# Performance work log

Hardware: AMD Instinct MI355X
Metric: run time of the kernel (lower is better)

Reference implementation:

```python
import jax, jax.numpy as jnp
import numpy as np

N = 100000      # nodes
E = 1600000     # edges (before self-loops)
IN = 256        # input features
HID = 128       # hidden channels
HEADS = 8
C = HID // HEADS  # per-head channels = 16
L = 3           # num GAT layers
EPS = 1e-5      # batchnorm eps
NEG_SLOPE = 0.2 # leaky relu slope (PyG GATConv default)


def setup_inputs() -> dict:
    key = jax.random.key(0)
    ks = jax.random.split(key, 8)
    s = 0.05
    x = jax.random.normal(ks[0], (N, IN), jnp.float32)
    edge_index = jax.random.randint(ks[1], (2, E), 0, N, dtype=jnp.int32)
    proj_w = jax.random.normal(ks[2], (IN, HID), jnp.float32) * s
    proj_b = jnp.zeros((HID,), jnp.float32)
    W = jax.random.normal(ks[3], (L, HID, HID), jnp.float32) * s
    att_src = jax.random.normal(ks[4], (L, HEADS, C), jnp.float32) * s
    att_dst = jax.random.normal(ks[5], (L, HEADS, C), jnp.float32) * s
    conv_b = jnp.zeros((L, HID), jnp.float32)
    bn_g = jnp.ones((L, HID), jnp.float32)
    bn_b = jnp.zeros((L, HID), jnp.float32)
    fc_w = jax.random.normal(ks[6], (HID, 1), jnp.float32) * s
    fc_b = jnp.zeros((1,), jnp.float32)
    return {"x": x, "edge_index": edge_index, "proj_w": proj_w, "proj_b": proj_b,
            "W": W, "att_src": att_src, "att_dst": att_dst, "conv_b": conv_b,
            "bn_g": bn_g, "bn_b": bn_b, "fc_w": fc_w, "fc_b": fc_b}


def _gat_layer(x, src, dst, W, a_src, a_dst, b):
    # x: [N, HID] -> per-head features h: [N, HEADS, C]
    h = (x @ W).reshape(N, HEADS, C)
    al_src = jnp.einsum('nhc,hc->nh', h, a_src)  # [N, HEADS]
    al_dst = jnp.einsum('nhc,hc->nh', h, a_dst)  # [N, HEADS]
    e = jax.nn.leaky_relu(al_src[src] + al_dst[dst], NEG_SLOPE)  # [Etot, HEADS]
    # segment softmax over edges grouped by destination node
    m = jax.ops.segment_max(e, dst, num_segments=N)              # [N, HEADS]
    w = jnp.exp(e - m[dst])
    denom = jax.ops.segment_sum(w, dst, num_segments=N)          # [N, HEADS]
    alpha = w / (denom[dst] + 1e-16)                             # [Etot, HEADS]
    msg = h[src] * alpha[:, :, None]                             # [Etot, HEADS, C]
    out = jax.ops.segment_sum(msg, dst, num_segments=N)          # [N, HEADS, C]
    return out.reshape(N, HID) + b


def reference(x, edge_index, proj_w, proj_b, W, att_src, att_dst, conv_b, bn_g, bn_b, fc_w, fc_b):
    # add self loops (PyG GATConv default)
    loops = jnp.arange(N, dtype=edge_index.dtype)
    src = jnp.concatenate([edge_index[0], loops])
    dst = jnp.concatenate([edge_index[1], loops])
    h = jax.nn.elu(x @ proj_w + proj_b)
    for i in range(L):
        res = h
        h = _gat_layer(h, src, dst, W[i], att_src[i], att_dst[i], conv_b[i])
        mu = h.mean(axis=0)
        var = h.var(axis=0)  # biased, matches torch BN training math
        h = (h - mu) / jnp.sqrt(var + EPS) * bn_g[i] + bn_b[i]
        h = jax.nn.elu(h)
        h = h + res  # residual; dropout is identity in eval mode
    return h @ fc_w + fc_b
```

## Files before the change

kernel.cpp:

```cpp
#include <hip/hip_runtime.h>
#include <hip/hip_bf16.h>

#define NN 100000
#define EE 1600000
#define ETOT (NN + EE)
#define HID 128
#define HEADS 8
#define CH 16
#define EPS_BN 1e-5f
#define NEG_SLOPE 0.2f
#define NB 196
#define NBLK_A 208

typedef unsigned short ushort_t;
typedef unsigned int uint_t;
typedef __attribute__((ext_vector_type(8))) short short8;
typedef __attribute__((ext_vector_type(4))) float float4v;

__device__ inline uint_t f2bf(float x) {
    __hip_bfloat16 b = __float2bfloat16(x);
    return (uint_t)*reinterpret_cast<unsigned short*>(&b);
}
__device__ inline uint_t pack2(float lo, float hi) {
    return f2bf(lo) | (f2bf(hi) << 16);
}
__device__ inline float bf_lo(uint_t u) { return __uint_as_float(u << 16); }
__device__ inline float bf_hi(uint_t u) { return __uint_as_float(u & 0xffff0000u); }

__global__ __launch_bounds__(256) void bucket_hist(const int* __restrict__ ei,
                                                   int* bcnt, int* lbase) {
    __shared__ int h[256];
    int t = threadIdx.x;
    h[t] = 0;
    __syncthreads();
    int base = blockIdx.x * 8192;
    #pragma unroll 4
    for (int j = 0; j < 32; ++j) {
        int i = base + j * 256 + t;
        if (i < ETOT) {
            int d = (i < EE) ? ei[EE + i] : (i - EE);
            atomicAdd(&h[d >> 9], 1);
        }
    }
    __syncthreads();
    if (t < NB) {
        int v = h[t];
        lbase[blockIdx.x * NB + t] = v ? atomicAdd(&bcnt[t], v) : 0;
    }
}

__global__ void bucket_scan(const int* __restrict__ bcnt, int* bbase, int* rowptr) {
    __shared__ int s[256];
    int t = threadIdx.x;
    int orig = (t < NB) ? bcnt[t] : 0;
    s[t] = orig;
    __syncthreads();
    for (int off = 1; off < 256; off <<= 1) {
        int add = (t >= off) ? s[t - off] : 0;
        __syncthreads();
        s[t] += add;
        __syncthreads();
    }
    if (t < NB) bbase[t] = s[t] - orig;
    if (t == 0) { bbase[NB] = ETOT; rowptr[NN] = ETOT; }
}

__global__ __launch_bounds__(256) void bucket_scatter(const int* __restrict__ ei,
                                                      const int* __restrict__ bbase,
                                                      const int* __restrict__ lbase,
                                                      uint_t* __restrict__ pairs) {
    __shared__ uint_t spair[8192];
    __shared__ unsigned char sbk[8192];
    __shared__ int h[256];
    __shared__ int lscan[256];
    __shared__ int sbase[256];
    int t = threadIdx.x;
    int base = blockIdx.x * 8192;
    int nloc = ETOT - base; if (nloc > 8192) nloc = 8192;
    sbase[t] = (t < NB) ? (bbase[t] + lbase[blockIdx.x * NB + t]) : 0;
    h[t] = 0;
    __syncthreads();
    #pragma unroll 4
    for (int j = 0; j < 32; ++j) {
        int i = base + j * 256 + t;
        if (i < ETOT) {
            int d = (i < EE) ? ei[EE + i] : (i - EE);
            atomicAdd(&h[d >> 9], 1);
        }
    }
    __syncthreads();
    int orig = h[t];
    lscan[t] = orig;
    __syncthreads();
    for (int off = 1; off < 256; off <<= 1) {
        int add = (t >= off) ? lscan[t - off] : 0;
        __syncthreads();
        lscan[t] += add;
        __syncthreads();
    }
    int excl = lscan[t] - orig;
    __syncthreads();
    lscan[t] = excl;
    h[t] = excl;
    __syncthreads();
    #pragma unroll 4
    for (int j = 0; j < 32; ++j) {
        int i = base + j * 256 + t;
        if (i < ETOT) {
            int sv, dv;
            if (i < EE) { sv = ei[i]; dv = ei[EE + i]; }
            else        { sv = i - EE; dv = sv; }
            int bk = dv >> 9;
            int lp = atomicAdd(&h[bk], 1);
            spair[lp] = ((uint_t)sv << 9) | (uint_t)(dv & 511);
            sbk[lp] = (unsigned char)bk;
        }
    }
    __syncthreads();
    #pragma unroll 4
    for (int j = 0; j < 32; ++j) {
        int i = j * 256 + t;
        if (i < nloc) {
            int bk = sbk[i];
            pairs[sbase[bk] + (i - lscan[bk])] = spair[i];
        }
    }
}

__global__ __launch_bounds__(256) void bucket_build(const uint_t* __restrict__ pairs,
                                                    const int* __restrict__ bbase,
                                                    int* __restrict__ rowptr,
                                                    int* __restrict__ csrc) {
    __shared__ int cnt[512];
    __shared__ int cur[512];
    int b = blockIdx.x;
    int t = threadIdx.x;
    int lo = b << 9;
    int nn = NN - lo; if (nn > 512) nn = 512;
    int e0 = bbase[b];
    int e1 = bbase[b + 1];
    cnt[t] = 0; cnt[t + 256] = 0;
    __syncthreads();
    for (int i = e0 + t; i < e1; i += 256)
        atomicAdd(&cnt[pairs[i] & 511], 1);
    __syncthreads();
    int oc0 = cnt[t], oc1 = cnt[t + 256];
    for (int off = 1; off < 512; off <<= 1) {
        int i0 = t, i1 = t + 256;
        int a0 = cnt[i0] + ((i0 >= off) ? cnt[i0 - off] : 0);
        int a1 = cnt[i1] + ((i1 >= off) ? cnt[i1 - off] : 0);
        __syncthreads();
        cnt[i0] = a0; cnt[i1] = a1;
        __syncthreads();
    }
    int ex0 = cnt[t] - oc0, ex1 = cnt[t + 256] - oc1;
    __syncthreads();
    cur[t] = e0 + ex0; cur[t + 256] = e0 + ex1;
    if (t < nn)       rowptr[lo + t] = e0 + ex0;
    if (t + 256 < nn) rowptr[lo + 256 + t] = e0 + ex1;
    __syncthreads();
    for (int i = e0 + t; i < e1; i += 256) {
        uint_t p = pairs[i];
        int pos = atomicAdd(&cur[p & 511], 1);
        csrc[pos] = (int)(p >> 9);
    }
}


__global__ void castw(const float* __restrict__ proj_w, const float* __restrict__ W,
                      ushort_t* __restrict__ pwT, ushort_t* __restrict__ WT) {
    int id = blockIdx.x * 256 + threadIdx.x;
    if (id < 32768) {
        int n = id >> 8, k = id & 255;
        pwT[id] = (ushort_t)f2bf(proj_w[k * 128 + n]);
    } else if (id < 81920) {
        int id2 = id - 32768;
        int l = id2 >> 14, r = id2 & 16383;
        int n = r >> 7, k = r & 127;
        WT[id2] = (ushort_t)f2bf(W[l * 16384 + k * 128 + n]);
    }
}


__global__ __launch_bounds__(256) void gemm_mfma(
    const void* __restrict__ Aptr, int mode,
    const ushort_t* __restrict__ Bt, int K,
    const float* __restrict__ bias, ushort_t* __restrict__ Cb,
    const float* __restrict__ a_src, const float* __restrict__ a_dst,
    float* __restrict__ al_s, float* __restrict__ al_d, int M,
    uint_t* __restrict__ hbio, const float* __restrict__ stats,
    const float* __restrict__ bn_gl, const float* __restrict__ bn_bl)
{
    __shared__ uint4 smem[2304];
    __shared__ float2 scsh[128];
    ushort_t* As = (ushort_t*)smem;
    ushort_t* Bs = As + 128 * 72;

    int t = threadIdx.x;
    int row0 = blockIdx.x * 128;
    int lane = t & 63, wv = t >> 6;
    int wm = wv >> 1, wn = wv & 1;
    int lr = lane & 15, quad = lane >> 4;

    if (mode == 2 && t < 128) {
        float mu = stats[t] * (1.0f / NN);
        float var = stats[128 + t] * (1.0f / NN) - mu * mu;
        float s = bn_gl[t] * rsqrtf(var + EPS_BN);
        scsh[t] = make_float2(s, bn_bl[t] - mu * s);
    }
    __syncthreads();

    float4v acc[4][4] = {};

    for (int k0 = 0; k0 < K; k0 += 64) {
        if (mode == 1) {
            const float* A = (const float*)Aptr;
            #pragma unroll
            for (int j = 0; j < 8; ++j) {
                int idx = j * 256 + t;
                int row = idx >> 4;
                int c4 = (idx & 15) * 4;
                int gr = row0 + row;
                float4 v = make_float4(0.f, 0.f, 0.f, 0.f);
                if (gr < M) v = *(const float4*)(A + (size_t)gr * K + k0 + c4);
                uint2 u; u.x = pack2(v.x, v.y); u.y = pack2(v.z, v.w);
                *(uint2*)&As[row * 72 + c4] = u;
            }
        } else if (mode == 0) {
            const ushort_t* A = (const ushort_t*)Aptr;
            #pragma unroll
            for (int j = 0; j < 4; ++j) {
                int idx = j * 256 + t;
                int row = idx >> 3;
                int c8 = (idx & 7) * 8;
                int gr = row0 + row;
                uint4 v = make_uint4(0, 0, 0, 0);
                if (gr < M) v = *(const uint4*)(A + (size_t)gr * K + k0 + c8);
                *(uint4*)&As[row * 72 + c8] = v;
            }
        } else {
            const uint_t* agg = (const uint_t*)Aptr;
            #pragma unroll
            for (int j = 0; j < 4; ++j) {
                int idx = j * 256 + t;
                int row = idx >> 3;
                int u4 = idx & 7;
                int gr = row0 + row;
                uint4 o = make_uint4(0, 0, 0, 0);
                if (gr < M) {
                    size_t gi = (size_t)gr * 64 + (k0 >> 1) + u4 * 4;
                    uint4 av = *(const uint4*)(agg + gi);
                    uint4 rv = *(const uint4*)(hbio + gi);
                    int cb = k0 + u4 * 8;
                    uint_t aa[4] = {av.x, av.y, av.z, av.w};
                    uint_t rr[4] = {rv.x, rv.y, rv.z, rv.w};
                    float ov[8];
                    #pragma unroll
                    for (int q = 0; q < 4; ++q) {
                        float2 s0 = scsh[cb + 2 * q];
                        float2 s1 = scsh[cb + 2 * q + 1];
                        float x0 = s0.x * bf_lo(aa[q]) + s0.y;
                        x0 = x0 > 0.f ? x0 : __expf(x0) - 1.f;
                        x0 += bf_lo(rr[q]);
                        float x1 = s1.x * bf_hi(aa[q]) + s1.y;
                        x1 = x1 > 0.f ? x1 : __expf(x1) - 1.f;
                        x1 += bf_hi(rr[q]);
                        ov[2 * q] = x0; ov[2 * q + 1] = x1;
                    }
                    o.x = pack2(ov[0], ov[1]); o.y = pack2(ov[2], ov[3]);
                    o.z = pack2(ov[4], ov[5]); o.w = pack2(ov[6], ov[7]);
                    *(uint4*)(hbio + gi) = o;
                }
                *(uint4*)&As[row * 72 + u4 * 8] = o;
            }
        }
        #pragma unroll
        for (int j = 0; j < 4; ++j) {
            int idx = j * 256 + t;
            int row = idx >> 3;
            int c8 = (idx & 7) * 8;
            uint4 v = *(const uint4*)(Bt + (size_t)row * K + k0 + c8);
            *(uint4*)&Bs[row * 72 + c8] = v;
        }
        __syncthreads();

        const ushort_t* Ab = As + (wm * 64 + lr) * 72 + quad * 8;
        const ushort_t* Bb = Bs + (wn * 64 + lr) * 72 + quad * 8;
        #pragma unroll
        for (int ks = 0; ks < 64; ks += 32) {
            short8 a[4], b[4];
            #pragma unroll
            for (int ti = 0; ti < 4; ++ti) a[ti] = *(const short8*)(Ab + ti * 16 * 72 + ks);
            #pragma unroll
            for (int tj = 0; tj < 4; ++tj) b[tj] = *(const short8*)(Bb + tj * 16 * 72 + ks);
            #pragma unroll
            for (int ti = 0; ti < 4; ++ti)
                #pragma unroll
                for (int tj = 0; tj < 4; ++tj)
                    acc[ti][tj] = __builtin_amdgcn_mfma_f32_16x16x32_bf16(
                        a[ti], b[tj], acc[ti][tj], 0, 0, 0);
        }
        __syncthreads();
    }

    float* sc = (float*)smem;
    for (int ti = 0; ti < 4; ++ti) {
        #pragma unroll
        for (int tj = 0; tj < 4; ++tj) {
            #pragma unroll
            for (int r = 0; r < 4; ++r) {
                int rloc = wm * 16 + quad * 4 + r;
                int col = wn * 64 + tj * 16 + lr;
                sc[rloc * 132 + col] = acc[ti][tj][r];
            }
        }
        __syncthreads();
        #pragma unroll
        for (int j = 0; j < 4; ++j) {
            int idx = j * 256 + t;
            int row = idx >> 5;
            int c4 = (idx & 31) * 4;
            float4 v = *(const float4*)&sc[row * 132 + c4];
            int gr = row0 + (row >> 4) * 64 + ti * 16 + (row & 15);
            if (gr < M) {
                if (bias) {
                    float4 bv = *(const float4*)(bias + c4);
                    v.x += bv.x; v.y += bv.y; v.z += bv.z; v.w += bv.w;
                    v.x = v.x > 0.f ? v.x : __expf(v.x) - 1.f;
                    v.y = v.y > 0.f ? v.y : __expf(v.y) - 1.f;
                    v.z = v.z > 0.f ? v.z : __expf(v.z) - 1.f;
                    v.w = v.w > 0.f ? v.w : __expf(v.w) - 1.f;
                }
                uint2 u; u.x = pack2(v.x, v.y); u.y = pack2(v.z, v.w);
                *(uint2*)(Cb + (size_t)gr * 128 + c4) = u;
            }
        }
        if (al_s) {
            int row = t & 31, head = t >> 5;
            int gr = row0 + (row >> 4) * 64 + ti * 16 + (row & 15);
            if (gr < M) {
                const float* rp = &sc[row * 132 + head * 16];
                const float* spv = a_src + head * 16;
                const float* dpv = a_dst + head * 16;
                float s1 = 0.f, s2 = 0.f;
                #pragma unroll
                for (int c = 0; c < 16; ++c) {
                    float hv = rp[c];
                    s1 += hv * spv[c];
                    s2 += hv * dpv[c];
                }
                al_s[gr * 8 + head] = s1;
                al_d[gr * 8 + head] = s2;
            }
        }
        __syncthreads();
    }
}


__global__ __launch_bounds__(256) void gat_agg(
    const int* __restrict__ rowptr, const int* __restrict__ csrc,
    const uint_t* __restrict__ h2b, const float* __restrict__ al_s,
    const float* __restrict__ al_d, const float* __restrict__ bias,
    uint_t* __restrict__ outb)
{
    int wv = (blockIdx.x * blockDim.x + threadIdx.x) >> 6;
    int lane = threadIdx.x & 63;
    if (wv >= NN) return;
    int e0 = rowptr[wv], e1 = rowptr[wv + 1];
    int head = lane >> 3;
    int ch = lane * 2;
    float ald = al_d[wv * HEADS + head];
    float acc0 = 0.f, acc1 = 0.f, denom = 0.f;

    int e = e0;
    for (; e + 8 <= e1; e += 8) {
        int ss[8]; float aa[8]; uint_t pp[8];
        #pragma unroll
        for (int k = 0; k < 8; ++k) ss[k] = csrc[e + k];
        #pragma unroll
        for (int k = 0; k < 8; ++k) aa[k] = al_s[ss[k] * HEADS + head];
        #pragma unroll
        for (int k = 0; k < 8; ++k) pp[k] = h2b[(size_t)ss[k] * 64 + lane];
        #pragma unroll
        for (int k = 0; k < 8; ++k) {
            float x = aa[k] + ald;
            x = fmaxf(x, NEG_SLOPE * x);
            float w = __expf(x);
            acc0 += w * bf_lo(pp[k]);
            acc1 += w * bf_hi(pp[k]);
            denom += w;
        }
    }
    for (; e < e1; ++e) {
        int s = csrc[e];
        float a = al_s[s * HEADS + head];
        uint_t p = h2b[(size_t)s * 64 + lane];
        float x = a + ald;
        x = fmaxf(x, NEG_SLOPE * x);
        float w = __expf(x);
        acc0 += w * bf_lo(p);
        acc1 += w * bf_hi(p);
        denom += w;
    }
    float inv = 1.0f / (denom + 1e-16f);
    outb[(size_t)wv * 64 + lane] = pack2(acc0 * inv + bias[ch], acc1 * inv + bias[ch + 1]);
}


__global__ void bn_stats(const uint_t* __restrict__ ab, float* stats) {
    int t = threadIdx.x;
    int u_idx = t >> 1, hi = t & 1;
    float s = 0.f, q = 0.f;
    for (int r = blockIdx.x; r < NN; r += gridDim.x) {
        uint_t u = ab[(size_t)r * 64 + u_idx];
        float v = hi ? bf_hi(u) : bf_lo(u);
        s += v;
        q += v * v;
    }
    atomicAdd(&stats[t], s);
    atomicAdd(&stats[HID + t], q);
}


__global__ __launch_bounds__(256) void fc_fused(
    const uint_t* __restrict__ aggb, const uint_t* __restrict__ hb,
    const float* __restrict__ stats, const float* __restrict__ g,
    const float* __restrict__ be, const float* __restrict__ w,
    const float* __restrict__ fb, float* __restrict__ out)
{
    __shared__ float2 scsh[128];
    int t = threadIdx.x;
    if (t < 128) {
        float mu = stats[t] * (1.0f / NN);
        float var = stats[128 + t] * (1.0f / NN) - mu * mu;
        float s = g[t] * rsqrtf(var + EPS_BN);
        scsh[t] = make_float2(s, be[t] - mu * s);
    }
    __syncthreads();
    int wv = (blockIdx.x * 256 + t) >> 6;
    int lane = t & 63;
    if (wv >= NN) return;
    uint_t av = aggb[(size_t)wv * 64 + lane];
    uint_t rv = hb[(size_t)wv * 64 + lane];
    int c = lane * 2;
    float2 s0 = scsh[c], s1 = scsh[c + 1];
    float x0 = s0.x * bf_lo(av) + s0.y;
    x0 = x0 > 0.f ? x0 : __expf(x0) - 1.f;
    x0 += bf_lo(rv);
    float x1 = s1.x * bf_hi(av) + s1.y;
    x1 = x1 > 0.f ? x1 : __expf(x1) - 1.f;
    x1 += bf_hi(rv);
    float2 wl = *(const float2*)(w + c);
    float acc = x0 * wl.x + x1 * wl.y;
    #pragma unroll
    for (int off = 32; off > 0; off >>= 1)
        acc += __shfl_down(acc, off, 64);
    if (lane == 0) out[wv] = acc + fb[0];
}


extern "C" void kernel_launch(void* const* d_in, const int* in_sizes, int n_in,
                              void* d_out, int out_size, void* d_ws, size_t ws_size,
                              hipStream_t stream) {
    const float* x       = (const float*)d_in[0];
    const int*   ei      = (const int*)  d_in[1];
    const float* proj_w  = (const float*)d_in[2];
    const float* proj_b  = (const float*)d_in[3];
    const float* W       = (const float*)d_in[4];
    const float* att_src = (const float*)d_in[5];
    const float* att_dst = (const float*)d_in[6];
    const float* conv_b  = (const float*)d_in[7];
    const float* bn_g    = (const float*)d_in[8];
    const float* bn_b    = (const float*)d_in[9];
    const float* fc_w    = (const float*)d_in[10];
    const float* fc_b    = (const float*)d_in[11];
    float* out = (float*)d_out;

    char* p = (char*)d_ws;
    uint_t*   hb   = (uint_t*)p;   p += (size_t)NN * 64 * 4;
    uint_t*   h2b  = (uint_t*)p;   p += (size_t)NN * 64 * 4;
    uint_t*   aggb = (uint_t*)p;   p += (size_t)NN * 64 * 4;
    uint_t*   pairs = (uint_t*)aggb;
    float*    al_s = (float*)p;    p += (size_t)NN * HEADS * 4;
    float*    al_d = (float*)p;    p += (size_t)NN * HEADS * 4;
    int* rowptr    = (int*)p;      p += ((size_t)(NN + 1) * 4 + 255) & ~255ull;
    int* csrc      = (int*)p;      p += (size_t)ETOT * 4;
    int* bcnt      = (int*)p;      p += 1024;
    float* stats3  = (float*)p;    p += 3 * 1024;
    int* bbase     = (int*)p;      p += 1024;
    int* lbase     = (int*)p;      p += (size_t)NBLK_A * NB * 4 + 256;
    ushort_t* pwT  = (ushort_t*)p; p += 128 * 256 * 2;
    ushort_t* WT   = (ushort_t*)p; p += 3 * 128 * 128 * 2;
    (void)ws_size; (void)n_in; (void)in_sizes; (void)out_size;

    hipMemsetAsync(bcnt, 0, 4096, stream);

    castw<<<320, 256, 0, stream>>>(proj_w, W, pwT, WT);

    gemm_mfma<<<(NN + 127) / 128, 256, 0, stream>>>(
        x, 1, pwT, 256, proj_b, (ushort_t*)hb, nullptr, nullptr, nullptr, nullptr, NN,
        nullptr, nullptr, nullptr, nullptr);

    bucket_hist<<<NBLK_A, 256, 0, stream>>>(ei, bcnt, (int*)lbase);
    bucket_scan<<<1, 256, 0, stream>>>(bcnt, bbase, rowptr);
    bucket_scatter<<<NBLK_A, 256, 0, stream>>>(ei, bbase, (const int*)lbase, pairs);
    bucket_build<<<NB, 256, 0, stream>>>(pairs, bbase, rowptr, csrc);

    for (int l = 0; l < 3; ++l) {
        const ushort_t* WTl = WT + (size_t)l * 128 * 128;
        const float* asl = att_src + (size_t)l * HEADS * CH;
        const float* adl = att_dst + (size_t)l * HEADS * CH;
        const float* cbl = conv_b + (size_t)l * HID;
        float* stl = stats3 + l * 256;

        if (l == 0) {
            gemm_mfma<<<(NN + 127) / 128, 256, 0, stream>>>(
                hb, 0, WTl, 128, nullptr, (ushort_t*)h2b, asl, adl, al_s, al_d, NN,
                nullptr, nullptr, nullptr, nullptr);
        } else {
            gemm_mfma<<<(NN + 127) / 128, 256, 0, stream>>>(
                aggb, 2, WTl, 128, nullptr, (ushort_t*)h2b, asl, adl, al_s, al_d, NN,
                hb, stats3 + (l - 1) * 256, bn_g + (size_t)(l - 1) * HID,
                bn_b + (size_t)(l - 1) * HID);
        }
        gat_agg<<<(NN + 3) / 4, 256, 0, stream>>>(rowptr, csrc, h2b, al_s, al_d, cbl, aggb);
        bn_stats<<<512, 128, 0, stream>>>(aggb, stl);
    }

    fc_fused<<<(NN + 3) / 4, 256, 0, stream>>>(
        aggb, hb, stats3 + 2 * 256, bn_g + 2 * HID, bn_b + 2 * HID, fc_w, fc_b, out);
}
```

Measured before the change: 836.7 us.

## Split wavefront across two edges in GAT aggregation and batch GEMM epilogue

The aggregation kernel now has each half-wavefront process a different edge, with every lane loading 8 bytes (four bf16 channels) instead of 4. The partial sums are combined with a cross-half shuffle. Attention logits are pre-scaled by log2(e) in the GEMM epilogue so that exp2f can replace __expf. The GEMM epilogue now writes two 16-row tiles per barrier round instead of one, and bn_stats unrolls its row loop by four. The separate memset is folded into the castw kernel to remove one launch. The combined changes aim to cut per-edge instruction overhead and raise memory-level parallelism in the gather, at the cost of a shuffle reduction and idle lanes on odd-length tails.

```diff
diff --git a/kernel.cpp b/kernel.cpp
--- a/kernel.cpp
+++ b/kernel.cpp
@@ -9,6 +9,7 @@
 #define CH 16
 #define EPS_BN 1e-5f
 #define NEG_SLOPE 0.2f
+#define LOG2E 1.4426950408889634f
 #define NB 196
 #define NBLK_A 208
 
@@ -26,6 +27,7 @@
 }
 __device__ inline float bf_lo(uint_t u) { return __uint_as_float(u << 16); }
 __device__ inline float bf_hi(uint_t u) { return __uint_as_float(u & 0xffff0000u); }
+
 
 __global__ __launch_bounds__(256) void bucket_hist(const int* __restrict__ ei,
                                                    int* bcnt, int* lbase) {
@@ -168,8 +170,10 @@
 
 
 __global__ void castw(const float* __restrict__ proj_w, const float* __restrict__ W,
-                      ushort_t* __restrict__ pwT, ushort_t* __restrict__ WT) {
+                      ushort_t* __restrict__ pwT, ushort_t* __restrict__ WT,
+                      int* __restrict__ zbuf) {
     int id = blockIdx.x * 256 + threadIdx.x;
+    if (id < 1024) zbuf[id] = 0;
     if (id < 32768) {
         int n = id >> 8, k = id & 255;
         pwT[id] = (ushort_t)f2bf(proj_w[k * 128 + n]);
@@ -304,24 +308,28 @@
     }
 
     float* sc = (float*)smem;
-    for (int ti = 0; ti < 4; ++ti) {
-        #pragma unroll
-        for (int tj = 0; tj < 4; ++tj) {
-            #pragma unroll
-            for (int r = 0; r < 4; ++r) {
-                int rloc = wm * 16 + quad * 4 + r;
-                int col = wn * 64 + tj * 16 + lr;
-                sc[rloc * 132 + col] = acc[ti][tj][r];
-            }
-        }
-        __syncthreads();
-        #pragma unroll
-        for (int j = 0; j < 4; ++j) {
+    for (int tp = 0; tp < 2; ++tp) {
+        #pragma unroll
+        for (int th = 0; th < 2; ++th) {
+            int ti = tp * 2 + th;
+            #pragma unroll
+            for (int tj = 0; tj < 4; ++tj) {
+                #pragma unroll
+                for (int r = 0; r < 4; ++r) {
+                    int rloc = wm * 32 + th * 16 + quad * 4 + r;
+                    int col = wn * 64 + tj * 16 + lr;
+                    sc[rloc * 132 + col] = acc[ti][tj][r];
+                }
+            }
+        }
+        __syncthreads();
+        #pragma unroll
+        for (int j = 0; j < 8; ++j) {
             int idx = j * 256 + t;
             int row = idx >> 5;
             int c4 = (idx & 31) * 4;
             float4 v = *(const float4*)&sc[row * 132 + c4];
-            int gr = row0 + (row >> 4) * 64 + ti * 16 + (row & 15);
+            int gr = row0 + (row >> 5) * 64 + tp * 32 + (row & 31);
             if (gr < M) {
                 if (bias) {
                     float4 bv = *(const float4*)(bias + c4);
@@ -336,21 +344,25 @@
             }
         }
         if (al_s) {
-            int row = t & 31, head = t >> 5;
-            int gr = row0 + (row >> 4) * 64 + ti * 16 + (row & 15);
-            if (gr < M) {
-                const float* rp = &sc[row * 132 + head * 16];
-                const float* spv = a_src + head * 16;
-                const float* dpv = a_dst + head * 16;
-                float s1 = 0.f, s2 = 0.f;
-                #pragma unroll
-                for (int c = 0; c < 16; ++c) {
-                    float hv = rp[c];
-                    s1 += hv * spv[c];
-                    s2 += hv * dpv[c];
+            #pragma unroll
+            for (int jj = 0; jj < 2; ++jj) {
+                int task = jj * 256 + t;
+                int row = task & 63, head = task >> 6;
+                int gr = row0 + (row >> 5) * 64 + tp * 32 + (row & 31);
+                if (gr < M) {
+                    const float* rp = &sc[row * 132 + head * 16];
+                    const float* spv = a_src + head * 16;
+                    const float* dpv = a_dst + head * 16;
+                    float s1 = 0.f, s2 = 0.f;
+                    #pragma unroll
+                    for (int c = 0; c < 16; ++c) {
+                        float hv = rp[c];
+                        s1 += hv * spv[c];
+                        s2 += hv * dpv[c];
+                    }
+                    al_s[gr * 8 + head] = s1 * LOG2E;
+                    al_d[gr * 8 + head] = s2 * LOG2E;
                 }
-                al_s[gr * 8 + head] = s1;
-                al_d[gr * 8 + head] = s2;
             }
         }
         __syncthreads();
@@ -360,51 +372,68 @@
 
 __global__ __launch_bounds__(256) void gat_agg(
     const int* __restrict__ rowptr, const int* __restrict__ csrc,
-    const uint_t* __restrict__ h2b, const float* __restrict__ al_s,
+    const uint2* __restrict__ h2b2, const float* __restrict__ al_s,
     const float* __restrict__ al_d, const float* __restrict__ bias,
-    uint_t* __restrict__ outb)
+    uint2* __restrict__ outb2)
 {
     int wv = (blockIdx.x * blockDim.x + threadIdx.x) >> 6;
     int lane = threadIdx.x & 63;
     if (wv >= NN) return;
+    int eh = lane >> 5;
+    int ln = lane & 31;
+    int head = ln >> 2;
     int e0 = rowptr[wv], e1 = rowptr[wv + 1];
-    int head = lane >> 3;
-    int ch = lane * 2;
-    float ald = al_d[wv * HEADS + head];
-    float acc0 = 0.f, acc1 = 0.f, denom = 0.f;
+    float ald = al_d[wv * 8 + head];
+    float a0 = 0.f, a1 = 0.f, a2 = 0.f, a3 = 0.f, denom = 0.f;
 
     int e = e0;
     for (; e + 8 <= e1; e += 8) {
-        int ss[8]; float aa[8]; uint_t pp[8];
-        #pragma unroll
-        for (int k = 0; k < 8; ++k) ss[k] = csrc[e + k];
-        #pragma unroll
-        for (int k = 0; k < 8; ++k) aa[k] = al_s[ss[k] * HEADS + head];
-        #pragma unroll
-        for (int k = 0; k < 8; ++k) pp[k] = h2b[(size_t)ss[k] * 64 + lane];
-        #pragma unroll
-        for (int k = 0; k < 8; ++k) {
+        int ss[4]; float aa[4]; uint2 pp[4];
+        #pragma unroll
+        for (int k = 0; k < 4; ++k) ss[k] = csrc[e + 2 * k + eh];
+        #pragma unroll
+        for (int k = 0; k < 4; ++k) aa[k] = al_s[ss[k] * 8 + head];
+        #pragma unroll
+        for (int k = 0; k < 4; ++k) pp[k] = h2b2[(size_t)ss[k] * 32 + ln];
+        #pragma unroll
+        for (int k = 0; k < 4; ++k) {
             float x = aa[k] + ald;
             x = fmaxf(x, NEG_SLOPE * x);
-            float w = __expf(x);
-            acc0 += w * bf_lo(pp[k]);
-            acc1 += w * bf_hi(pp[k]);
+            float w = exp2f(x);
+            a0 += w * bf_lo(pp[k].x);
+            a1 += w * bf_hi(pp[k].x);
+            a2 += w * bf_lo(pp[k].y);
+            a3 += w * bf_hi(pp[k].y);
             denom += w;
         }
     }
-    for (; e < e1; ++e) {
-        int s = csrc[e];
-        float a = al_s[s * HEADS + head];
-        uint_t p = h2b[(size_t)s * 64 + lane];
+    for (; e < e1; e += 2) {
+        bool valid = (e + eh) < e1;
+        int s = csrc[valid ? e + eh : e];
+        float a = al_s[s * 8 + head];
+        uint2 p = h2b2[(size_t)s * 32 + ln];
         float x = a + ald;
         x = fmaxf(x, NEG_SLOPE * x);
-        float w = __expf(x);
-        acc0 += w * bf_lo(p);
-        acc1 += w * bf_hi(p);
+        float w = valid ? exp2f(x) : 0.f;
+        a0 += w * bf_lo(p.x);
+        a1 += w * bf_hi(p.x);
+        a2 += w * bf_lo(p.y);
+        a3 += w * bf_hi(p.y);
         denom += w;
     }
-    float inv = 1.0f / (denom + 1e-16f);
-    outb[(size_t)wv * 64 + lane] = pack2(acc0 * inv + bias[ch], acc1 * inv + bias[ch + 1]);
+    a0 += __shfl_xor(a0, 32, 64);
+    a1 += __shfl_xor(a1, 32, 64);
+    a2 += __shfl_xor(a2, 32, 64);
+    a3 += __shfl_xor(a3, 32, 64);
+    denom += __shfl_xor(denom, 32, 64);
+    if (eh == 0) {
+        float inv = 1.0f / (denom + 1e-16f);
+        int c = ln * 4;
+        uint2 o;
+        o.x = pack2(a0 * inv + bias[c],     a1 * inv + bias[c + 1]);
+        o.y = pack2(a2 * inv + bias[c + 2], a3 * inv + bias[c + 3]);
+        outb2[(size_t)wv * 32 + ln] = o;
+    }
 }
 
 
@@ -412,11 +441,17 @@
     int t = threadIdx.x;
     int u_idx = t >> 1, hi = t & 1;
     float s = 0.f, q = 0.f;
-    for (int r = blockIdx.x; r < NN; r += gridDim.x) {
-        uint_t u = ab[(size_t)r * 64 + u_idx];
-        float v = hi ? bf_hi(u) : bf_lo(u);
-        s += v;
-        q += v * v;
+    for (int r0 = blockIdx.x * 4; r0 < NN; r0 += gridDim.x * 4) {
+        #pragma unroll
+        for (int j = 0; j < 4; ++j) {
+            int r = r0 + j;
+            if (r < NN) {
+                uint_t u = ab[(size_t)r * 64 + u_idx];
+                float v = hi ? bf_hi(u) : bf_lo(u);
+                s += v;
+                q += v * v;
+            }
+        }
     }
     atomicAdd(&stats[t], s);
     atomicAdd(&stats[HID + t], q);
@@ -494,9 +529,7 @@
     ushort_t* WT   = (ushort_t*)p; p += 3 * 128 * 128 * 2;
     (void)ws_size; (void)n_in; (void)in_sizes; (void)out_size;
 
-    hipMemsetAsync(bcnt, 0, 4096, stream);
-
-    castw<<<320, 256, 0, stream>>>(proj_w, W, pwT, WT);
+    castw<<<320, 256, 0, stream>>>(proj_w, W, pwT, WT, bcnt);
 
     gemm_mfma<<<(NN + 127) / 128, 256, 0, stream>>>(
         x, 1, pwT, 256, proj_b, (ushort_t*)hb, nullptr, nullptr, nullptr, nullptr, NN,
@@ -524,7 +557,8 @@
                 hb, stats3 + (l - 1) * 256, bn_g + (size_t)(l - 1) * HID,
                 bn_b + (size_t)(l - 1) * HID);
         }
-        gat_agg<<<(NN + 3) / 4, 256, 0, stream>>>(rowptr, csrc, h2b, al_s, al_d, cbl, aggb);
+        gat_agg<<<(NN + 3) / 4, 256, 0, stream>>>(
+            rowptr, csrc, (const uint2*)h2b, al_s, al_d, cbl, (uint2*)aggb);
         bn_stats<<<512, 128, 0, stream>>>(aggb, stl);
     }
 
```

Result: faster. 819.0 us (-2.1%).
